# Kernel tuning notes

Measured on AMD Instinct MI355X. Metric: run time of the kernel, lower is better.

Reference implementation:

```python
import jax, jax.numpy as jnp
import numpy as np

IMG_H = IMG_W = 640
NUM_CLASSES = 80
B = 8
NUM_ANCHORS = 76725
MAX_TOTAL = 200          # max_total_size == max_size_per_class
SCORE_TH = 0.5
IOU_TH = 0.5
K_CAND = 256             # per-class candidate pool for NMS (>= max survivors)
VARIANCES = jnp.asarray([0.1, 0.1, 0.2, 0.2], jnp.float32)


def _build_anchors(img_h, img_w):
    # RetinaNet AnchorBox: levels 3..7, 3 ratios x 3 scales, [cx, cy, w, h]
    ratios = [0.5, 1.0, 2.0]
    scales = [2.0 ** x for x in (0.0, 1.0 / 3.0, 2.0 / 3.0)]
    areas = [s * s for s in (32.0, 64.0, 128.0, 256.0, 512.0)]
    out = []
    for lvl, stride in enumerate([2 ** i for i in range(3, 8)]):
        dims = []
        for r in ratios:
            h = np.sqrt(areas[lvl] / r)
            w = areas[lvl] / h
            for s in scales:
                dims.append([w * s, h * s])
        dims = np.asarray(dims, np.float32)                      # [9,2]
        fh = int(np.ceil(img_h / stride)); fw = int(np.ceil(img_w / stride))
        rx = (np.arange(fw, dtype=np.float32) + 0.5) * stride
        ry = (np.arange(fh, dtype=np.float32) + 0.5) * stride
        cx, cy = np.meshgrid(rx, ry)
        centers = np.broadcast_to(np.stack([cx, cy], -1)[:, :, None, :], (fh, fw, 9, 2))
        d = np.broadcast_to(dims[None, None], (fh, fw, 9, 2))
        out.append(np.concatenate([centers, d], -1).reshape(-1, 4))
    return jnp.asarray(np.concatenate(out, 0))                   # [A,4]


def setup_inputs() -> dict:
    key = jax.random.key(0)
    k1, k2 = jax.random.split(key)
    box_pred = jax.random.normal(k1, (B, NUM_ANCHORS, 4), jnp.float32)
    cls_pred = jax.random.normal(k2, (B, NUM_ANCHORS, NUM_CLASSES), jnp.float32)
    anchor_boxes = _build_anchors(IMG_H, IMG_W)
    return {"box_pred": box_pred, "cls_pred": cls_pred, "anchor_boxes": anchor_boxes}


def _iou_one_vs_many(box, boxes):
    # box [4] vs boxes [K,4] in corner format
    lt = jnp.maximum(box[:2], boxes[:, :2])
    rb = jnp.minimum(box[2:], boxes[:, 2:])
    wh = jnp.maximum(rb - lt, 0.0)
    inter = wh[:, 0] * wh[:, 1]
    a1 = (box[2] - box[0]) * (box[3] - box[1])
    a2 = (boxes[:, 2] - boxes[:, 0]) * (boxes[:, 3] - boxes[:, 1])
    return inter / jnp.maximum(a1 + a2 - inter, 1e-8)


def _nms_keep(boxes, scores):
    # boxes [K,4] already sorted by descending score; greedy NMS
    eligible = scores > SCORE_TH
    idx = jnp.arange(K_CAND)

    def body(i, keep):
        iou = _iou_one_vs_many(boxes[i], boxes)
        suppress = (iou > IOU_TH) & (idx > i)
        return jnp.where(keep[i], keep & ~suppress, keep)

    keep = jax.lax.fori_loop(0, K_CAND, body, eligible)
    keep = keep & ((jnp.cumsum(keep) - 1) < MAX_TOTAL)           # max_size_per_class cap
    return keep


def _decode_and_nms(box_pred, cls_pred, anchor_boxes):
    scores_all = jax.nn.sigmoid(cls_pred)                        # [B,A,C]
    # decode: (dx,dy,dw,dh)*variances against [cx,cy,w,h] anchors
    d = box_pred * VARIANCES
    xy = d[..., :2] * anchor_boxes[None, :, 2:] + anchor_boxes[None, :, :2]
    wh = jnp.exp(d[..., 2:]) * anchor_boxes[None, :, 2:]
    boxes = jnp.concatenate([xy - 0.5 * wh, xy + 0.5 * wh], -1)  # [B,A,4] corners

    sc = jnp.swapaxes(scores_all, 1, 2)                          # [B,C,A]
    top_sc, top_idx = jax.lax.top_k(sc, K_CAND)                  # [B,C,K] sorted desc
    cand_boxes = jnp.take_along_axis(boxes[:, None], top_idx[..., None], axis=2)  # [B,C,K,4]

    keep = jax.lax.stop_gradient(jax.vmap(jax.vmap(_nms_keep))(cand_boxes, top_sc))  # [B,C,K]
    sel = jnp.where(keep, top_sc, -1.0)

    flat_sc = sel.reshape(B, -1)                                 # [B,C*K]
    flat_boxes = cand_boxes.reshape(B, -1, 4)
    flat_lbl = jnp.broadcast_to(jnp.arange(NUM_CLASSES)[None, :, None],
                                (B, NUM_CLASSES, K_CAND)).reshape(B, -1)

    fs, fi = jax.lax.top_k(flat_sc, MAX_TOTAL)                   # combine across classes
    out_boxes = jnp.take_along_axis(flat_boxes, fi[..., None], axis=1)
    out_lbl = jnp.take_along_axis(flat_lbl, fi, axis=1).astype(jnp.float32)
    valid = fs > 0.0                                             # pad invalid slots
    return (jnp.where(valid[..., None], out_boxes, 0.0),
            jnp.where(valid, fs, 0.0),
            jnp.where(valid, out_lbl, -1.0))


def reference(box_pred, cls_pred, anchor_boxes):
    return _decode_and_nms(box_pred, cls_pred, anchor_boxes)
```

## Files before the change

kernel.cpp:

```cpp
#include <hip/hip_runtime.h>
#include <math.h>
#include <stdint.h>

typedef unsigned long long u64;
typedef unsigned int u32;

#define NB 8
#define NA 76725
#define NC 80
#define KC 256
#define MAXT 200
#define CAP 2048
#define SELCAP 768
#define TAU 2.0f
#define CHUNK 512
#define NCHUNK 150
#define BCAP 48
#define CSTRIDE 16

#define OFF_BUFA      0ull
#define OFF_CLASSLIST 10485760ull
#define OFF_CANDBOX   11796480ull
#define OFF_COUNTS    14417920ull

__device__ __forceinline__ void kf_proc(float4 v, int i, int a0,
                                        u64 (*bucket)[BCAP], u32* bcnt) {
  int a = a0 + i / (NC / 4);
  int c0 = (i % (NC / 4)) * 4;
  float vv[4] = {v.x, v.y, v.z, v.w};
#pragma unroll
  for (int j = 0; j < 4; j++) {
    if (vv[j] > TAU) {
      int c = c0 + j;
      u32 pos = atomicAdd(&bcnt[c], 1u);
      if (pos < BCAP)
        bucket[c][pos] = ((u64)__float_as_uint(vv[j]) << 32) | (u32)a;
    }
  }
}

__global__ __launch_bounds__(256) void kfilter(const float* __restrict__ cls,
                                               u64* __restrict__ bufA,
                                               u32* __restrict__ counts) {
  __shared__ u64 bucket[NC][BCAP];
  __shared__ u32 bcnt[NC];
  __shared__ u32 gbase[NC];
  __shared__ u32 pref[NC + 1];

  const int b = blockIdx.x / NCHUNK;
  const int ch = blockIdx.x % NCHUNK;
  const int tid = threadIdx.x;
  const int a0 = ch * CHUNK;
  const int aN = (NA - a0) < CHUNK ? (NA - a0) : CHUNK;

  for (int i = tid; i < NC; i += 256) bcnt[i] = 0;
  __syncthreads();

  const float4* p = (const float4*)(cls + ((size_t)b * NA + a0) * NC);
  const int n4 = aN * (NC / 4);
  for (int i0 = tid; i0 < n4; i0 += 2048) {
    float4 v[8];
    bool g[8];
#pragma unroll
    for (int u = 0; u < 8; u++) {
      g[u] = (i0 + u * 256) < n4;
      if (g[u]) v[u] = p[i0 + u * 256];
    }
#pragma unroll
    for (int u = 0; u < 8; u++)
      if (g[u]) kf_proc(v[u], i0 + u * 256, a0, bucket, bcnt);
  }
  __syncthreads();
  if (tid < NC) {
    u32 n = bcnt[tid];
    if (n > BCAP) n = BCAP;
    bcnt[tid] = n;
    gbase[tid] = atomicAdd(&counts[(b * NC + tid) * CSTRIDE], n);
  }
  __syncthreads();
  if (tid == 0) {
    u32 s = 0;
    for (int c = 0; c < NC; c++) { pref[c] = s; s += bcnt[c]; }
    pref[NC] = s;
  }
  __syncthreads();
  const int total = (int)pref[NC];
  for (int e = tid; e < total; e += 256) {
    int lo = 0, hi = NC;
    while (lo + 1 < hi) { int mid = (lo + hi) >> 1; if ((int)pref[mid] <= e) lo = mid; else hi = mid; }
    int c = lo;
    int loc = e - (int)pref[c];
    u32 gb = gbase[c] + (u32)loc;
    if (gb < CAP)
      bufA[((size_t)(b * NC + c)) * CAP + gb] = bucket[c][loc];
  }
}

__global__ __launch_bounds__(256) void kselect(
    const float* __restrict__ cls, const float* __restrict__ boxp,
    const float* __restrict__ anc, u64* __restrict__ bufA,
    const u32* __restrict__ counts, u64* __restrict__ classList,
    float4* __restrict__ candBox) {
  __shared__ __align__(16) char smem[24576];
  u64* sbuf = (u64*)smem;
  u64 (*scolT)[KC] = (u64(*)[KC])smem;
  float4* sBox = (float4*)(smem + 8192);
  float* sAr = (float*)(smem + 12288);
  u32* hist = (u32*)(smem + 16384);
  u64* sel = (u64*)(smem + 16384);
  u64* skey = (u64*)(smem + 22528);
  __shared__ u32 sRowAnyLo[4], sRowAnyHi[4];
  __shared__ int sNsel, sExtra, sSb;

  const int tid = threadIdx.x;
  const int bc = blockIdx.x;
  const int b = bc / NC, c = bc % NC;
  u64* buf = bufA + (size_t)bc * CAP;

  int cnt0 = (int)counts[bc * CSTRIDE];
  if (cnt0 > CAP) cnt0 = CAP;
  int cnt = cnt0;
  if (cnt0 < KC) {
    if (tid == 0) sExtra = 0;
    __syncthreads();
    for (int a = tid; a < NA; a += 256) {
      float x = cls[((size_t)b * NA + a) * NC + c];
      if (x > 0.0f && !(x > TAU)) {
        int pos = cnt0 + atomicAdd(&sExtra, 1);
        if (pos < CAP) buf[pos] = ((u64)__float_as_uint(x) << 32) | (u32)a;
      }
    }
    __syncthreads();
    cnt = cnt0 + sExtra;
  }
  if (cnt > CAP) cnt = CAP;

  for (int i = tid; i < 1024; i += 256) hist[i] = 0;
  if (tid == 0) sNsel = 0;
  skey[tid] = 0;
  for (int e = tid; e < cnt; e += 256) sbuf[e] = buf[e];
  __syncthreads();

  for (int e = tid; e < cnt; e += 256) {
    float f = __uint_as_float((u32)(sbuf[e] >> 32));
    int bin = (int)(f * 170.0f);
    bin = bin < 0 ? 0 : (bin > 1023 ? 1023 : bin);
    atomicAdd(&hist[bin], 1u);
  }
  __syncthreads();

  if (tid < 64) {
    int s = 0;
#pragma unroll
    for (int i = 0; i < 16; i++) s += (int)hist[tid * 16 + i];
    int suf = s;
#pragma unroll
    for (int d = 1; d < 64; d <<= 1) {
      int t = __shfl_down(suf, d, 64);
      if (tid + d < 64) suf += t;
    }
    u64 mask = __ballot(suf >= KC);
    int sb = mask ? (63 - __clzll((long long)mask)) : 0;
    if (tid == 0) sSb = sb;
  }
  __syncthreads();
  const int sb = sSb;

  for (int e = tid; e < cnt; e += 256) {
    u64 k = sbuf[e];
    float f = __uint_as_float((u32)(k >> 32));
    int bin = (int)(f * 170.0f);
    bin = bin < 0 ? 0 : (bin > 1023 ? 1023 : bin);
    if ((bin >> 4) >= sb) {
      float sc = 1.0f / (1.0f + expf(-f));
      u32 a = (u32)k;
      int pos = atomicAdd(&sNsel, 1);
      if (pos < SELCAP)
        sel[pos] = ((u64)__float_as_uint(sc) << 32) | (0xFFFFFFFFu - a);
    }
  }
  __syncthreads();
  int nsel = sNsel;
  if (nsel > SELCAP) nsel = SELCAP;

  for (int e = tid; e < nsel; e += 256) {
    u64 k = sel[e];
    int r = 0;
    for (int q = 0; q < nsel; q++) r += (sel[q] > k) ? 1 : 0;
    if (r < KC) skey[r] = k;
  }
  __syncthreads();

  {
    if (tid < 4) { sRowAnyLo[tid] = 0; sRowAnyHi[tid] = 0; }
    u64 k = skey[tid];
    u32 a = 0xFFFFFFFFu - (u32)k;
    if (k == 0ull || a >= NA) a = 0;
    float4 p = ((const float4*)boxp)[(size_t)b * NA + a];
    float4 an = ((const float4*)anc)[a];
    float dx = __fmul_rn(p.x, 0.1f), dy = __fmul_rn(p.y, 0.1f);
    float dw = __fmul_rn(p.z, 0.2f), dh = __fmul_rn(p.w, 0.2f);
    float cx = __fadd_rn(__fmul_rn(dx, an.z), an.x);
    float cy = __fadd_rn(__fmul_rn(dy, an.w), an.y);
    float w = __fmul_rn(expf(dw), an.z);
    float h = __fmul_rn(expf(dh), an.w);
    float4 bx;
    bx.x = __fsub_rn(cx, __fmul_rn(0.5f, w));
    bx.y = __fsub_rn(cy, __fmul_rn(0.5f, h));
    bx.z = __fadd_rn(cx, __fmul_rn(0.5f, w));
    bx.w = __fadd_rn(cy, __fmul_rn(0.5f, h));
    sBox[tid] = bx;
    sAr[tid] = __fmul_rn(__fsub_rn(bx.z, bx.x), __fsub_rn(bx.w, bx.y));
    candBox[(size_t)bc * KC + tid] = bx;
  }
  __syncthreads();

  {
    const int j = tid;
    float4 bj = sBox[j];
    float aj = sAr[j];
    u64 cw[4] = {0ull, 0ull, 0ull, 0ull};
    for (int i = 0; i < j; i++) {
      float4 bi = sBox[i];
      float ai = sAr[i];
      float lx = fmaxf(bi.x, bj.x), ly = fmaxf(bi.y, bj.y);
      float rx = fminf(bi.z, bj.z), ry = fminf(bi.w, bj.w);
      float wx = fmaxf(__fsub_rn(rx, lx), 0.0f);
      float wy = fmaxf(__fsub_rn(ry, ly), 0.0f);
      float inter = __fmul_rn(wx, wy);
      float uni = fmaxf(__fsub_rn(__fadd_rn(ai, aj), inter), 1e-8f);
      float iou = __fdiv_rn(inter, uni);
      if (iou > 0.5f) cw[i >> 6] |= (1ull << (i & 63));
    }
#pragma unroll
    for (int w = 0; w < 4; w++) scolT[w][j] = cw[w];
#pragma unroll
    for (int w = 0; w < 4; w++) {
      u64 r = cw[w];
#pragma unroll
      for (int m = 1; m < 64; m <<= 1) {
        int lo = __shfl_xor((int)(u32)r, m, 64);
        int hi = __shfl_xor((int)(r >> 32), m, 64);
        r |= ((u64)(u32)hi << 32) | (u32)lo;
      }
      if ((tid & 63) == 0) {
        atomicOr(&sRowAnyLo[w], (u32)r);
        atomicOr(&sRowAnyHi[w], (u32)(r >> 32));
      }
    }
  }
  __syncthreads();

  if (tid < 64) {
    const int ln = tid;
    u64 C[4][4];
#pragma unroll
    for (int s = 0; s < 4; s++)
#pragma unroll
      for (int w = 0; w < 4; w++) C[s][w] = scolT[w][s * 64 + ln];
    int keep = 0;
#pragma unroll
    for (int s = 0; s < 4; s++)
      if (skey[s * 64 + ln] != 0ull) keep |= (1 << s);
#pragma unroll
    for (int w = 0; w < 4; w++) {
      u64 c0 = C[0][w], c1 = C[1][w], c2 = C[2][w], c3 = C[3][w];
      u64 rw = ((u64)sRowAnyHi[w] << 32) | (u64)sRowAnyLo[w];
      while (rw) {
        int t = __builtin_ctzll(rw);
        rw &= rw - 1;
        int kt = __shfl(keep, t, 64);
        if ((kt >> w) & 1) {
          int sup = (int)((c0 >> t) & 1) | ((int)((c1 >> t) & 1) << 1) |
                    ((int)((c2 >> t) & 1) << 2) | ((int)((c3 >> t) & 1) << 3);
          keep &= ~sup;
        }
      }
    }
    u64 m[4];
#pragma unroll
    for (int s = 0; s < 4; s++) m[s] = __ballot((keep >> s) & 1);
    int tot = 0;
#pragma unroll
    for (int s = 0; s < 4; s++) tot += __popcll(m[s]);
    int keptTotal = tot < MAXT ? tot : MAXT;
    u64 lmask = (1ull << ln) - 1ull;
    int base = 0;
#pragma unroll
    for (int s = 0; s < 4; s++) {
      int j = s * 64 + ln;
      int cum = base + (int)__popcll(m[s] & lmask);
      if (((keep >> s) & 1) && cum < MAXT) {
        u64 hi = skey[j] >> 32;
        classList[(size_t)bc * KC + cum] =
            (hi << 32) | (u64)(0xFFFFFFFFu - (u32)(c * KC + j));
      }
      base += (int)__popcll(m[s]);
    }
    for (int t2 = ln; t2 < KC; t2 += 64)
      if (t2 >= keptTotal) classList[(size_t)bc * KC + t2] = 0;
  }
}

__device__ __forceinline__ u64 shfl64(u64 v, int src) {
  int lo = __shfl((int)(u32)v, src, 64);
  int hi = __shfl((int)(v >> 32), src, 64);
  return ((u64)(u32)hi << 32) | (u32)lo;
}
__device__ __forceinline__ u64 shflxor64(u64 v, int mask) {
  int lo = __shfl_xor((int)(u32)v, mask, 64);
  int hi = __shfl_xor((int)(v >> 32), mask, 64);
  return ((u64)(u32)hi << 32) | (u32)lo;
}
#define CSWAP(a, b) { if ((a) < (b)) { u64 _t = (a); (a) = (b); (b) = _t; } }

__device__ __forceinline__ void wave_merge(u64 acc[4], const u64 cur[4], int ln) {
  u64 t0 = shfl64(cur[3], 63 - ln);
  u64 t1 = shfl64(cur[2], 63 - ln);
  u64 t2 = shfl64(cur[1], 63 - ln);
  u64 t3 = shfl64(cur[0], 63 - ln);
  acc[0] = acc[0] > t0 ? acc[0] : t0;
  acc[1] = acc[1] > t1 ? acc[1] : t1;
  acc[2] = acc[2] > t2 ? acc[2] : t2;
  acc[3] = acc[3] > t3 ? acc[3] : t3;
  CSWAP(acc[0], acc[2]); CSWAP(acc[1], acc[3]);
  CSWAP(acc[0], acc[1]); CSWAP(acc[2], acc[3]);
#pragma unroll
  for (int s = 32; s >= 1; s >>= 1) {
#pragma unroll
    for (int k = 0; k < 4; k++) {
      u64 o = shflxor64(acc[k], s);
      u64 mx = acc[k] > o ? acc[k] : o;
      u64 mn = acc[k] < o ? acc[k] : o;
      acc[k] = ((ln & s) == 0) ? mx : mn;
    }
  }
}

__global__ __launch_bounds__(256) void kmerge(const u64* __restrict__ classList,
                                              const float4* __restrict__ candBox,
                                              float* __restrict__ out) {
  __shared__ u64 lds[4 * KC];
  const int tid = threadIdx.x, b = blockIdx.x;
  const int w = tid >> 6, ln = tid & 63;
  const u64* base = classList + ((size_t)b * NC + w * 20) * KC;
  u64 acc[4];
#pragma unroll
  for (int k = 0; k < 4; k++) acc[k] = base[k * 64 + ln];
  for (int m = 1; m < 20; m++) {
    u64 cur[4];
#pragma unroll
    for (int k = 0; k < 4; k++) cur[k] = base[(size_t)m * KC + k * 64 + ln];
    wave_merge(acc, cur, ln);
  }
#pragma unroll
  for (int k = 0; k < 4; k++) lds[w * KC + k * 64 + ln] = acc[k];
  __syncthreads();
  if (w == 0) {
    for (int m = 1; m < 4; m++) {
      u64 cur[4];
#pragma unroll
      for (int k = 0; k < 4; k++) cur[k] = lds[m * KC + k * 64 + ln];
      wave_merge(acc, cur, ln);
    }
#pragma unroll
    for (int k = 0; k < 4; k++) lds[k * 64 + ln] = acc[k];
  }
  __syncthreads();
  if (tid < MAXT) {
    u64 k = lds[tid];
    float4 bx = make_float4(0.f, 0.f, 0.f, 0.f);
    float sc = 0.0f, lb = -1.0f;
    if (k != 0ull) {
      sc = __uint_as_float((u32)(k >> 32));
      u32 flat = 0xFFFFFFFFu - (u32)k;
      int cc = (int)(flat >> 8), kk = (int)(flat & 255u);
      bx = candBox[((size_t)b * NC + cc) * KC + kk];
      lb = (float)cc;
    }
    float* ob = out + ((size_t)b * MAXT + tid) * 4;
    ob[0] = bx.x; ob[1] = bx.y; ob[2] = bx.z; ob[3] = bx.w;
    out[NB * MAXT * 4 + b * MAXT + tid] = sc;
    out[NB * MAXT * 4 + NB * MAXT + b * MAXT + tid] = lb;
  }
}

extern "C" void kernel_launch(void* const* d_in, const int* in_sizes, int n_in,
                              void* d_out, int out_size, void* d_ws,
                              size_t ws_size, hipStream_t stream) {
  const float* boxp = (const float*)d_in[0];
  const float* cls = (const float*)d_in[1];
  const float* anc = (const float*)d_in[2];
  char* ws = (char*)d_ws;
  u64* bufA = (u64*)(ws + OFF_BUFA);
  u64* classList = (u64*)(ws + OFF_CLASSLIST);
  float4* candBox = (float4*)(ws + OFF_CANDBOX);
  u32* counts = (u32*)(ws + OFF_COUNTS);

  hipMemsetAsync(counts, 0, NB * NC * CSTRIDE * sizeof(u32), stream);
  kfilter<<<NB * NCHUNK, 256, 0, stream>>>(cls, bufA, counts);
  kselect<<<NB * NC, 256, 0, stream>>>(cls, boxp, anc, bufA, counts, classList,
                                       candBox);
  kmerge<<<NB, 256, 0, stream>>>(classList, candBox, (float*)d_out);
}
```

Measured before the change: 372.5 us.

## Raise filter threshold, shrink buffers, and load-balance IoU mask computation

The filter kernel now stores only logits above a higher threshold into smaller per-class buckets and a smaller global buffer. This cuts global writes and the memory footprint, and the fallback path rescans the class column at the original threshold when too few candidates survive. In the select kernel, the triangular IoU loop is split so each thread gets a balanced pair of segments and writes its bits with atomicOr, and the rank-sort inner loop is unrolled by 8. The fallback rescans of the class column cost more whenever a class has fewer stored candidates than the pool size.

```diff
diff --git a/kernel.cpp b/kernel.cpp
--- a/kernel.cpp
+++ b/kernel.cpp
@@ -11,17 +11,19 @@
 #define KC 256
 #define MAXT 200
 #define CAP 2048
+#define TCAP 1024
 #define SELCAP 768
 #define TAU 2.0f
+#define TAU_STORE 2.5f
 #define CHUNK 512
 #define NCHUNK 150
-#define BCAP 48
+#define BCAP 32
 #define CSTRIDE 16
 
 #define OFF_BUFA      0ull
-#define OFF_CLASSLIST 10485760ull
-#define OFF_CANDBOX   11796480ull
-#define OFF_COUNTS    14417920ull
+#define OFF_CLASSLIST 5242880ull
+#define OFF_CANDBOX   6553600ull
+#define OFF_COUNTS    9175040ull
 
 __device__ __forceinline__ void kf_proc(float4 v, int i, int a0,
                                         u64 (*bucket)[BCAP], u32* bcnt) {
@@ -30,7 +32,7 @@
   float vv[4] = {v.x, v.y, v.z, v.w};
 #pragma unroll
   for (int j = 0; j < 4; j++) {
-    if (vv[j] > TAU) {
+    if (vv[j] > TAU_STORE) {
       int c = c0 + j;
       u32 pos = atomicAdd(&bcnt[c], 1u);
       if (pos < BCAP)
@@ -91,14 +93,30 @@
     int c = lo;
     int loc = e - (int)pref[c];
     u32 gb = gbase[c] + (u32)loc;
-    if (gb < CAP)
-      bufA[((size_t)(b * NC + c)) * CAP + gb] = bucket[c][loc];
-  }
+    if (gb < TCAP)
+      bufA[((size_t)(b * NC + c)) * TCAP + gb] = bucket[c][loc];
+  }
+}
+
+__device__ __forceinline__ int logit_bin(u64 k) {
+  float f = __uint_as_float((u32)(k >> 32));
+  int bin = (int)(f * 170.0f);
+  return bin < 0 ? 0 : (bin > 1023 ? 1023 : bin);
+}
+
+__device__ __forceinline__ bool iou_gt(float4 bi, float ai, float4 bj, float aj) {
+  float lx = fmaxf(bi.x, bj.x), ly = fmaxf(bi.y, bj.y);
+  float rx = fminf(bi.z, bj.z), ry = fminf(bi.w, bj.w);
+  float wx = fmaxf(__fsub_rn(rx, lx), 0.0f);
+  float wy = fmaxf(__fsub_rn(ry, ly), 0.0f);
+  float inter = __fmul_rn(wx, wy);
+  float uni = fmaxf(__fsub_rn(__fadd_rn(ai, aj), inter), 1e-8f);
+  return __fdiv_rn(inter, uni) > 0.5f;
 }
 
 __global__ __launch_bounds__(256) void kselect(
     const float* __restrict__ cls, const float* __restrict__ boxp,
-    const float* __restrict__ anc, u64* __restrict__ bufA,
+    const float* __restrict__ anc, const u64* __restrict__ bufA,
     const u32* __restrict__ counts, u64* __restrict__ classList,
     float4* __restrict__ candBox) {
   __shared__ __align__(16) char smem[24576];
@@ -115,38 +133,44 @@
   const int tid = threadIdx.x;
   const int bc = blockIdx.x;
   const int b = bc / NC, c = bc % NC;
-  u64* buf = bufA + (size_t)bc * CAP;
-
-  int cnt0 = (int)counts[bc * CSTRIDE];
-  if (cnt0 > CAP) cnt0 = CAP;
-  int cnt = cnt0;
-  if (cnt0 < KC) {
-    if (tid == 0) sExtra = 0;
+  const u64* buf = bufA + (size_t)bc * TCAP;
+
+  int cntT = (int)counts[bc * CSTRIDE];
+  if (cntT > TCAP) cntT = TCAP;
+
+  for (int i = tid; i < 1024; i += 256) hist[i] = 0;
+  if (tid == 0) { sNsel = 0; sExtra = 0; }
+  skey[tid] = 0;
+
+  int cnt;
+  if (cntT >= KC) {
+    cnt = cntT;
+    for (int e = tid; e < cnt; e += 256) sbuf[e] = buf[e];
+  } else {
     __syncthreads();
     for (int a = tid; a < NA; a += 256) {
       float x = cls[((size_t)b * NA + a) * NC + c];
-      if (x > 0.0f && !(x > TAU)) {
-        int pos = cnt0 + atomicAdd(&sExtra, 1);
-        if (pos < CAP) buf[pos] = ((u64)__float_as_uint(x) << 32) | (u32)a;
+      if (x > TAU) {
+        int pos = atomicAdd(&sExtra, 1);
+        if (pos < CAP) sbuf[pos] = ((u64)__float_as_uint(x) << 32) | (u32)a;
       }
     }
     __syncthreads();
-    cnt = cnt0 + sExtra;
-  }
-  if (cnt > CAP) cnt = CAP;
-
-  for (int i = tid; i < 1024; i += 256) hist[i] = 0;
-  if (tid == 0) sNsel = 0;
-  skey[tid] = 0;
-  for (int e = tid; e < cnt; e += 256) sbuf[e] = buf[e];
-  __syncthreads();
-
-  for (int e = tid; e < cnt; e += 256) {
-    float f = __uint_as_float((u32)(sbuf[e] >> 32));
-    int bin = (int)(f * 170.0f);
-    bin = bin < 0 ? 0 : (bin > 1023 ? 1023 : bin);
-    atomicAdd(&hist[bin], 1u);
-  }
+    if (sExtra < KC) {
+      for (int a = tid; a < NA; a += 256) {
+        float x = cls[((size_t)b * NA + a) * NC + c];
+        if (x > 0.0f && !(x > TAU)) {
+          int pos = atomicAdd(&sExtra, 1);
+          if (pos < CAP) sbuf[pos] = ((u64)__float_as_uint(x) << 32) | (u32)a;
+        }
+      }
+      __syncthreads();
+    }
+    cnt = sExtra < CAP ? sExtra : CAP;
+  }
+  __syncthreads();
+
+  for (int e = tid; e < cnt; e += 256) atomicAdd(&hist[logit_bin(sbuf[e])], 1u);
   __syncthreads();
 
   if (tid < 64) {
@@ -168,25 +192,32 @@
 
   for (int e = tid; e < cnt; e += 256) {
     u64 k = sbuf[e];
-    float f = __uint_as_float((u32)(k >> 32));
-    int bin = (int)(f * 170.0f);
-    bin = bin < 0 ? 0 : (bin > 1023 ? 1023 : bin);
-    if ((bin >> 4) >= sb) {
+    if ((logit_bin(k) >> 4) >= sb) {
+      float f = __uint_as_float((u32)(k >> 32));
       float sc = 1.0f / (1.0f + expf(-f));
-      u32 a = (u32)k;
       int pos = atomicAdd(&sNsel, 1);
       if (pos < SELCAP)
-        sel[pos] = ((u64)__float_as_uint(sc) << 32) | (0xFFFFFFFFu - a);
+        sel[pos] = ((u64)__float_as_uint(sc) << 32) | (0xFFFFFFFFu - (u32)k);
     }
   }
   __syncthreads();
   int nsel = sNsel;
   if (nsel > SELCAP) nsel = SELCAP;
 
+#pragma unroll
+  for (int w = 0; w < 4; w++) scolT[w][tid] = 0ull;
   for (int e = tid; e < nsel; e += 256) {
     u64 k = sel[e];
     int r = 0;
-    for (int q = 0; q < nsel; q++) r += (sel[q] > k) ? 1 : 0;
+    int q = 0;
+    const int nful = nsel & ~7;
+    for (; q < nful; q += 8) {
+      u64 t0 = sel[q],     t1 = sel[q + 1], t2 = sel[q + 2], t3 = sel[q + 3];
+      u64 t4 = sel[q + 4], t5 = sel[q + 5], t6 = sel[q + 6], t7 = sel[q + 7];
+      r += (t0 > k) + (t1 > k) + (t2 > k) + (t3 > k) +
+           (t4 > k) + (t5 > k) + (t6 > k) + (t7 > k);
+    }
+    for (; q < nsel; q++) r += sel[q] > k;
     if (r < KC) skey[r] = k;
   }
   __syncthreads();
@@ -216,32 +247,52 @@
   __syncthreads();
 
   {
-    const int j = tid;
-    float4 bj = sBox[j];
-    float aj = sAr[j];
-    u64 cw[4] = {0ull, 0ull, 0ull, 0ull};
-    for (int i = 0; i < j; i++) {
-      float4 bi = sBox[i];
-      float ai = sAr[i];
-      float lx = fmaxf(bi.x, bj.x), ly = fmaxf(bi.y, bj.y);
-      float rx = fminf(bi.z, bj.z), ry = fminf(bi.w, bj.w);
-      float wx = fmaxf(__fsub_rn(rx, lx), 0.0f);
-      float wy = fmaxf(__fsub_rn(ry, ly), 0.0f);
-      float inter = __fmul_rn(wx, wy);
-      float uni = fmaxf(__fsub_rn(__fadd_rn(ai, aj), inter), 1e-8f);
-      float iou = __fdiv_rn(inter, uni);
-      if (iou > 0.5f) cw[i >> 6] |= (1ull << (i & 63));
-    }
-#pragma unroll
-    for (int w = 0; w < 4; w++) scolT[w][j] = cw[w];
+    auto proc_seg = [&](int j, int ibeg, int iend) {
+      float4 bj = sBox[j];
+      float aj = sAr[j];
+#pragma unroll
+      for (int w = 0; w < 4; w++) {
+        int lo = ibeg > (w << 6) ? ibeg : (w << 6);
+        int hi = iend < ((w + 1) << 6) ? iend : ((w + 1) << 6);
+        u64 bits = 0ull;
+        int i = lo;
+        for (; i + 3 < hi; i += 4) {
+          float4 b0 = sBox[i], b1 = sBox[i + 1], b2 = sBox[i + 2], b3 = sBox[i + 3];
+          float a0 = sAr[i], a1 = sAr[i + 1], a2 = sAr[i + 2], a3 = sAr[i + 3];
+          bits |= (u64)iou_gt(b0, a0, bj, aj) << (i & 63);
+          bits |= (u64)iou_gt(b1, a1, bj, aj) << ((i + 1) & 63);
+          bits |= (u64)iou_gt(b2, a2, bj, aj) << ((i + 2) & 63);
+          bits |= (u64)iou_gt(b3, a3, bj, aj) << ((i + 3) & 63);
+        }
+        for (; i < hi; i++)
+          bits |= (u64)iou_gt(sBox[i], sAr[i], bj, aj) << (i & 63);
+        if (bits) {
+          u32* p = (u32*)&scolT[w][j];
+          u32 blo = (u32)bits, bhi = (u32)(bits >> 32);
+          if (blo) atomicOr(p, blo);
+          if (bhi) atomicOr(p + 1, bhi);
+        }
+      }
+    };
+    const int u = tid & 127, h = tid >> 7;
+    if (h == 0) {
+      proc_seg(u, 0, u);
+      proc_seg(255 - u, 0, 128 - u);
+    } else {
+      proc_seg(255 - u, 128 - u, 255 - u);
+    }
+  }
+  __syncthreads();
+
+  {
 #pragma unroll
     for (int w = 0; w < 4; w++) {
-      u64 r = cw[w];
+      u64 r = scolT[w][tid];
 #pragma unroll
       for (int m = 1; m < 64; m <<= 1) {
-        int lo = __shfl_xor((int)(u32)r, m, 64);
-        int hi = __shfl_xor((int)(r >> 32), m, 64);
-        r |= ((u64)(u32)hi << 32) | (u32)lo;
+        int rlo = __shfl_xor((int)(u32)r, m, 64);
+        int rhi = __shfl_xor((int)(r >> 32), m, 64);
+        r |= ((u64)(u32)rhi << 32) | (u32)rlo;
       }
       if ((tid & 63) == 0) {
         atomicOr(&sRowAnyLo[w], (u32)r);
```

Result: faster. 358.7 us (-3.7%).
